# Kernel optimization log

Measured on AMD Instinct MI355X. Metric: run time of the kernel, lower is better.

The kernel has to match this reference:

```python
import jax, jax.numpy as jnp
import numpy as np

N_ATOMS = 20000
HIDDEN = 128
N_ITERS = 2
BATCH = 16
N_BONDS = 60000


def setup_inputs() -> dict:
    key = jax.random.key(0)
    k1, k2, k3, k4, k5, k6 = jax.random.split(key, 6)
    positions = jax.random.normal(k1, (BATCH, N_ATOMS, 3), dtype=jnp.float32)
    bonds = jax.random.randint(k2, (N_BONDS, 2), 0, N_ATOMS, dtype=jnp.int32)
    # nn.Linear(3, 128): weight [128,3], bias [128] -> store transposed for x @ W
    W_msg = jax.random.normal(k3, (3, HIDDEN), dtype=jnp.float32) / jnp.sqrt(3.0)
    b_msg = jax.random.normal(k4, (HIDDEN,), dtype=jnp.float32) * 0.01
    # nn.Linear(128, 3)
    W_upd = jax.random.normal(k5, (HIDDEN, 3), dtype=jnp.float32) / jnp.sqrt(float(HIDDEN))
    b_upd = jax.random.normal(k6, (3,), dtype=jnp.float32) * 0.01
    return {"positions": positions, "bonds": bonds,
            "W_msg": W_msg, "b_msg": b_msg, "W_upd": W_upd, "b_upd": b_upd}


def reference(positions, bonds, W_msg, b_msg, W_upd, b_upd):
    B, N, _ = positions.shape
    # Bidirectional edges: message flows src -> dst (adj_list[dst] contains src).
    src = jnp.concatenate([bonds[:, 0], bonds[:, 1]])  # [2E]
    dst = jnp.concatenate([bonds[:, 1], bonds[:, 0]])  # [2E]
    deg = jnp.zeros((N,), jnp.float32).at[dst].add(1.0)  # in-degree per atom
    inv_deg = jnp.where(deg > 0, 1.0 / jnp.maximum(deg, 1.0), 0.0)  # [N]

    h = positions
    for _ in range(N_ITERS):
        node_msg = h @ W_msg + b_msg                      # [B,N,H] msg_linear per node
        gathered = node_msg[:, src, :]                    # [B,2E,H]
        agg = jnp.zeros((B, N, HIDDEN), h.dtype).at[:, dst, :].add(gathered)  # sum per dst
        msgs = agg * inv_deg[None, :, None]               # mean over neighbors (0 if isolated)
        h = h + (msgs @ W_upd + b_upd)                    # update_linear + residual
    return h
```

## Files before the change

kernel.cpp:

```cpp
#include <hip/hip_runtime.h>

#define N_ATOMS 20000
#define BATCH   16
#define N_BONDS 60000
#define NB      (N_ATOMS * BATCH)
#define CAP     32

#define TRANS_BLOCKS 1250
#define DEG_BLOCKS   235
#define NGROUPS      1250

#define OFF_CNT   0
#define OFF_MC    20000
#define OFF_ADJF  20016
#define OFF_POST  (OFF_ADJF + N_ATOMS * CAP)
#define OFF_H2T   (OFF_POST + NB * 2)

__device__ __forceinline__ unsigned short f2bf(float f) {
    unsigned int u = __float_as_uint(f);
    u += 0x7FFFu + ((u >> 16) & 1u);
    return (unsigned short)(u >> 16);
}
__device__ __forceinline__ float bf2f(unsigned short h) {
    return __uint_as_float(((unsigned int)h) << 16);
}

__global__ void build_kernel(const float* __restrict__ pos, const int* __restrict__ bonds,
                             const float* __restrict__ W_msg, const float* __restrict__ b_msg,
                             const float* __restrict__ W_upd,
                             int* __restrict__ cnt, int* __restrict__ adjF,
                             float* __restrict__ Mc, ushort4* __restrict__ posT) {
    int blk = blockIdx.x;
    if (blk < TRANS_BLOCKS) {
        int t = blk * 256 + threadIdx.x;
        int b = t & 15, n = t >> 4;
        const float* p = pos + ((size_t)b * N_ATOMS + n) * 3;
        posT[n * 16 + b] = make_ushort4(f2bf(p[0]), f2bf(p[1]), f2bf(p[2]), 0);
    } else if (blk < TRANS_BLOCKS + DEG_BLOCKS) {
        int e = (blk - TRANS_BLOCKS) * 256 + threadIdx.x;
        if (e < N_BONDS) {
            int a0 = bonds[2 * e], a1 = bonds[2 * e + 1];
            int s0 = atomicAdd(&cnt[a0], 1);
            if (s0 < CAP) adjF[a0 * CAP + s0] = a1;
            int s1 = atomicAdd(&cnt[a1], 1);
            if (s1 < CAP) adjF[a1 * CAP + s1] = a0;
        }
    } else {
        int t = threadIdx.x;
        if (t < 12) {
            float s = 0.0f;
            if (t < 9) {
                int i = t / 3, j = t % 3;
                for (int k = 0; k < 128; ++k) s += W_msg[i * 128 + k] * W_upd[k * 3 + j];
            } else {
                int j = t - 9;
                for (int k = 0; k < 128; ++k) s += b_msg[k] * W_upd[k * 3 + j];
            }
            Mc[t] = s;
        }
    }
}

template <bool FINAL>
__global__ __launch_bounds__(256) void gather_kernel(const ushort4* __restrict__ hT,
                                                     const int* __restrict__ cnt,
                                                     const int* __restrict__ adjF,
                                                     const float* __restrict__ Mc,
                                                     const float* __restrict__ b_upd,
                                                     ushort4* __restrict__ outT,
                                                     float* __restrict__ outP) {
    __shared__ float lds[16 * 51];
    int t = threadIdx.x;
    int b = t & 15;
    int nl = t >> 4;
    int n = blockIdx.x * 16 + nl;
    const int4* al4 = (const int4*)(adjF + n * CAP);
    int dc = cnt[n];
    int d = dc > CAP ? CAP : dc;
    int4 ja = al4[0];
    int4 jb = al4[1];
    ushort4 mh = hT[n * 16 + b];
    float sx = 0.0f, sy = 0.0f, sz = 0.0f;
#define ACC(J) { ushort4 v = hT[(size_t)(J) * 16 + b]; \
                 sx += bf2f(v.x); sy += bf2f(v.y); sz += bf2f(v.z); }
    if (0 < d) ACC(ja.x)
    if (1 < d) ACC(ja.y)
    if (2 < d) ACC(ja.z)
    if (3 < d) ACC(ja.w)
    if (4 < d) ACC(jb.x)
    if (5 < d) ACC(jb.y)
    if (6 < d) ACC(jb.z)
    if (7 < d) ACC(jb.w)
    for (int k0 = 8; k0 < d; k0 += 8) {
        ja = al4[k0 >> 2];
        jb = al4[(k0 >> 2) + 1];
        if (k0 + 0 < d) ACC(ja.x)
        if (k0 + 1 < d) ACC(ja.y)
        if (k0 + 2 < d) ACC(ja.z)
        if (k0 + 3 < d) ACC(ja.w)
        if (k0 + 4 < d) ACC(jb.x)
        if (k0 + 5 < d) ACC(jb.y)
        if (k0 + 6 < d) ACC(jb.z)
        if (k0 + 7 < d) ACC(jb.w)
    }
#undef ACC
    float mex = bf2f(mh.x), mey = bf2f(mh.y), mez = bf2f(mh.z);
    float inv = d > 0 ? 1.0f / (float)d : 0.0f;
    float flag = d > 0 ? 1.0f : 0.0f;
    float o0 = mex + inv * (sx * Mc[0] + sy * Mc[3] + sz * Mc[6]) + flag * Mc[9]  + b_upd[0];
    float o1 = mey + inv * (sx * Mc[1] + sy * Mc[4] + sz * Mc[7]) + flag * Mc[10] + b_upd[1];
    float o2 = mez + inv * (sx * Mc[2] + sy * Mc[5] + sz * Mc[8]) + flag * Mc[11] + b_upd[2];
    if (!FINAL) {
        outT[n * 16 + b] = make_ushort4(f2bf(o0), f2bf(o1), f2bf(o2), 0);
    } else {
        lds[nl * 51 + b * 3 + 0] = o0;
        lds[nl * 51 + b * 3 + 1] = o1;
        lds[nl * 51 + b * 3 + 2] = o2;
        __syncthreads();
        int b2 = t >> 4, n2 = t & 15;
        float* op = outP + ((size_t)b2 * N_ATOMS + (size_t)(blockIdx.x * 16 + n2)) * 3;
        op[0] = lds[n2 * 51 + b2 * 3 + 0];
        op[1] = lds[n2 * 51 + b2 * 3 + 1];
        op[2] = lds[n2 * 51 + b2 * 3 + 2];
    }
}

extern "C" void kernel_launch(void* const* d_in, const int* in_sizes, int n_in,
                              void* d_out, int out_size, void* d_ws, size_t ws_size,
                              hipStream_t stream) {
    const float* positions = (const float*)d_in[0];
    const int* bonds = (const int*)d_in[1];
    const float* W_msg = (const float*)d_in[2];
    const float* b_msg = (const float*)d_in[3];
    const float* W_upd = (const float*)d_in[4];
    const float* b_upd = (const float*)d_in[5];
    float* out = (float*)d_out;

    int* wsi = (int*)d_ws;
    int* cnt = wsi + OFF_CNT;
    float* Mc = (float*)(wsi + OFF_MC);
    int* adjF = wsi + OFF_ADJF;
    ushort4* posT = (ushort4*)(wsi + OFF_POST);
    ushort4* h2T = (ushort4*)(wsi + OFF_H2T);

    hipMemsetAsync(cnt, 0, N_ATOMS * sizeof(int), stream);
    build_kernel<<<TRANS_BLOCKS + DEG_BLOCKS + 1, 256, 0, stream>>>(
        positions, bonds, W_msg, b_msg, W_upd, cnt, adjF, Mc, posT);
    gather_kernel<false><<<NGROUPS, 256, 0, stream>>>(posT, cnt, adjF, Mc, b_upd, h2T, nullptr);
    gather_kernel<true><<<NGROUPS, 256, 0, stream>>>(h2T, cnt, adjF, Mc, b_upd, nullptr, out);
}
```

Baseline: 38.50 us.

## Fuse two message-passing iterations into one 2-hop gather kernel

```diff
diff --git a/kernel.cpp b/kernel.cpp
--- a/kernel.cpp
+++ b/kernel.cpp
@@ -8,13 +8,11 @@
 
 #define TRANS_BLOCKS 1250
 #define DEG_BLOCKS   235
-#define NGROUPS      1250
 
 #define OFF_CNT   0
 #define OFF_MC    20000
-#define OFF_ADJF  20016
+#define OFF_ADJF  20024
 #define OFF_POST  (OFF_ADJF + N_ATOMS * CAP)
-#define OFF_H2T   (OFF_POST + NB * 2)
 
 __device__ __forceinline__ unsigned short f2bf(float f) {
     unsigned int u = __float_as_uint(f);
@@ -27,7 +25,7 @@
 
 __global__ void build_kernel(const float* __restrict__ pos, const int* __restrict__ bonds,
                              const float* __restrict__ W_msg, const float* __restrict__ b_msg,
-                             const float* __restrict__ W_upd,
+                             const float* __restrict__ W_upd, const float* __restrict__ b_upd,
                              int* __restrict__ cnt, int* __restrict__ adjF,
                              float* __restrict__ Mc, ushort4* __restrict__ posT) {
     int blk = blockIdx.x;
@@ -46,6 +44,7 @@
             if (s1 < CAP) adjF[a1 * CAP + s1] = a0;
         }
     } else {
+        __shared__ float sm[12];
         int t = threadIdx.x;
         if (t < 12) {
             float s = 0.0f;
@@ -56,73 +55,109 @@
                 int j = t - 9;
                 for (int k = 0; k < 128; ++k) s += b_msg[k] * W_upd[k * 3 + j];
             }
-            Mc[t] = s;
+            sm[t] = s;
+        }
+        __syncthreads();
+        if (t < 9) {
+            int i = t / 3, j = t % 3;
+            Mc[t] = sm[t];
+            float s = 0.0f;
+            for (int k = 0; k < 3; ++k) s += sm[i * 3 + k] * sm[k * 3 + j];
+            Mc[9 + t] = s;
+        } else if (t < 12) {
+            int j = t - 9;
+            float s = 0.0f;
+            for (int k = 0; k < 3; ++k) s += (sm[9 + k] + b_upd[k]) * sm[k * 3 + j];
+            Mc[18 + j] = s + 2.0f * sm[9 + j];
         }
     }
 }
 
-template <bool FINAL>
-__global__ __launch_bounds__(256) void gather_kernel(const ushort4* __restrict__ hT,
-                                                     const int* __restrict__ cnt,
-                                                     const int* __restrict__ adjF,
-                                                     const float* __restrict__ Mc,
-                                                     const float* __restrict__ b_upd,
-                                                     ushort4* __restrict__ outT,
-                                                     float* __restrict__ outP) {
-    __shared__ float lds[16 * 51];
+__global__ __launch_bounds__(128) void gather2_kernel(const ushort4* __restrict__ hT,
+                                                      const int* __restrict__ cnt,
+                                                      const int* __restrict__ adjF,
+                                                      const float* __restrict__ Mc,
+                                                      const float* __restrict__ b_upd,
+                                                      float* __restrict__ outP) {
+    __shared__ float lds[8 * 51];
     int t = threadIdx.x;
     int b = t & 15;
     int nl = t >> 4;
-    int n = blockIdx.x * 16 + nl;
+    int n = blockIdx.x * 8 + nl;
     const int4* al4 = (const int4*)(adjF + n * CAP);
-    int dc = cnt[n];
-    int d = dc > CAP ? CAP : dc;
+    int dn = cnt[n];
+    if (dn > CAP) dn = CAP;
     int4 ja = al4[0];
     int4 jb = al4[1];
     ushort4 mh = hT[n * 16 + b];
-    float sx = 0.0f, sy = 0.0f, sz = 0.0f;
-#define ACC(J) { ushort4 v = hT[(size_t)(J) * 16 + b]; \
-                 sx += bf2f(v.x); sy += bf2f(v.y); sz += bf2f(v.z); }
-    if (0 < d) ACC(ja.x)
-    if (1 < d) ACC(ja.y)
-    if (2 < d) ACC(ja.z)
-    if (3 < d) ACC(ja.w)
-    if (4 < d) ACC(jb.x)
-    if (5 < d) ACC(jb.y)
-    if (6 < d) ACC(jb.z)
-    if (7 < d) ACC(jb.w)
-    for (int k0 = 8; k0 < d; k0 += 8) {
-        ja = al4[k0 >> 2];
-        jb = al4[(k0 >> 2) + 1];
-        if (k0 + 0 < d) ACC(ja.x)
-        if (k0 + 1 < d) ACC(ja.y)
-        if (k0 + 2 < d) ACC(ja.z)
-        if (k0 + 3 < d) ACC(ja.w)
-        if (k0 + 4 < d) ACC(jb.x)
-        if (k0 + 5 < d) ACC(jb.y)
-        if (k0 + 6 < d) ACC(jb.z)
-        if (k0 + 7 < d) ACC(jb.w)
+    float S1x = 0.f, S1y = 0.f, S1z = 0.f;
+    float S2x = 0.f, S2y = 0.f, S2z = 0.f;
+    int js[8] = {ja.x, ja.y, ja.z, ja.w, jb.x, jb.y, jb.z, jb.w};
+#pragma unroll
+    for (int i = 0; i < 8; ++i) {
+        if (i < dn) {
+            int j = js[i];
+            int dj = cnt[j];
+            if (dj > CAP) dj = CAP;
+            const int4* jl4 = (const int4*)(adjF + j * CAP);
+            int4 ka = jl4[0];
+            int4 kb = jl4[1];
+            ushort4 hj = hT[(size_t)j * 16 + b];
+            S1x += bf2f(hj.x); S1y += bf2f(hj.y); S1z += bf2f(hj.z);
+            int ks[8] = {ka.x, ka.y, ka.z, ka.w, kb.x, kb.y, kb.z, kb.w};
+            float Tx = 0.f, Ty = 0.f, Tz = 0.f;
+#pragma unroll
+            for (int q = 0; q < 8; ++q) {
+                if (q < dj) {
+                    ushort4 hk = hT[(size_t)ks[q] * 16 + b];
+                    Tx += bf2f(hk.x); Ty += bf2f(hk.y); Tz += bf2f(hk.z);
+                }
+            }
+            for (int q = 8; q < dj; ++q) {
+                int kk = adjF[j * CAP + q];
+                ushort4 hk = hT[(size_t)kk * 16 + b];
+                Tx += bf2f(hk.x); Ty += bf2f(hk.y); Tz += bf2f(hk.z);
+            }
+            float invj = 1.0f / (float)dj;
+            S2x += invj * Tx; S2y += invj * Ty; S2z += invj * Tz;
+        }
     }
-#undef ACC
-    float mex = bf2f(mh.x), mey = bf2f(mh.y), mez = bf2f(mh.z);
-    float inv = d > 0 ? 1.0f / (float)d : 0.0f;
-    float flag = d > 0 ? 1.0f : 0.0f;
-    float o0 = mex + inv * (sx * Mc[0] + sy * Mc[3] + sz * Mc[6]) + flag * Mc[9]  + b_upd[0];
-    float o1 = mey + inv * (sx * Mc[1] + sy * Mc[4] + sz * Mc[7]) + flag * Mc[10] + b_upd[1];
-    float o2 = mez + inv * (sx * Mc[2] + sy * Mc[5] + sz * Mc[8]) + flag * Mc[11] + b_upd[2];
-    if (!FINAL) {
-        outT[n * 16 + b] = make_ushort4(f2bf(o0), f2bf(o1), f2bf(o2), 0);
-    } else {
-        lds[nl * 51 + b * 3 + 0] = o0;
-        lds[nl * 51 + b * 3 + 1] = o1;
-        lds[nl * 51 + b * 3 + 2] = o2;
-        __syncthreads();
-        int b2 = t >> 4, n2 = t & 15;
-        float* op = outP + ((size_t)b2 * N_ATOMS + (size_t)(blockIdx.x * 16 + n2)) * 3;
-        op[0] = lds[n2 * 51 + b2 * 3 + 0];
-        op[1] = lds[n2 * 51 + b2 * 3 + 1];
-        op[2] = lds[n2 * 51 + b2 * 3 + 2];
+    for (int i = 8; i < dn; ++i) {
+        int j = adjF[n * CAP + i];
+        int dj = cnt[j];
+        if (dj > CAP) dj = CAP;
+        ushort4 hj = hT[(size_t)j * 16 + b];
+        S1x += bf2f(hj.x); S1y += bf2f(hj.y); S1z += bf2f(hj.z);
+        float Tx = 0.f, Ty = 0.f, Tz = 0.f;
+        for (int q = 0; q < dj; ++q) {
+            int kk = adjF[j * CAP + q];
+            ushort4 hk = hT[(size_t)kk * 16 + b];
+            Tx += bf2f(hk.x); Ty += bf2f(hk.y); Tz += bf2f(hk.z);
+        }
+        float invj = 1.0f / (float)dj;
+        S2x += invj * Tx; S2y += invj * Ty; S2z += invj * Tz;
     }
+    float inv = dn > 0 ? 1.0f / (float)dn : 0.0f;
+    float flag = dn > 0 ? 1.0f : 0.0f;
+    float A1x = 2.f * S1x, A1y = 2.f * S1y, A1z = 2.f * S1z;
+    float o0 = bf2f(mh.x) + inv * (A1x * Mc[0] + A1y * Mc[3] + A1z * Mc[6]
+                                 + S2x * Mc[9] + S2y * Mc[12] + S2z * Mc[15])
+             + flag * Mc[18] + 2.f * b_upd[0];
+    float o1 = bf2f(mh.y) + inv * (A1x * Mc[1] + A1y * Mc[4] + A1z * Mc[7]
+                                 + S2x * Mc[10] + S2y * Mc[13] + S2z * Mc[16])
+             + flag * Mc[19] + 2.f * b_upd[1];
+    float o2 = bf2f(mh.z) + inv * (A1x * Mc[2] + A1y * Mc[5] + A1z * Mc[8]
+                                 + S2x * Mc[11] + S2y * Mc[14] + S2z * Mc[17])
+             + flag * Mc[20] + 2.f * b_upd[2];
+    lds[nl * 51 + b * 3 + 0] = o0;
+    lds[nl * 51 + b * 3 + 1] = o1;
+    lds[nl * 51 + b * 3 + 2] = o2;
+    __syncthreads();
+    int b2 = t >> 3, n2 = t & 7;
+    float* op = outP + ((size_t)b2 * N_ATOMS + (size_t)(blockIdx.x * 8 + n2)) * 3;
+    op[0] = lds[n2 * 51 + b2 * 3 + 0];
+    op[1] = lds[n2 * 51 + b2 * 3 + 1];
+    op[2] = lds[n2 * 51 + b2 * 3 + 2];
 }
 
 extern "C" void kernel_launch(void* const* d_in, const int* in_sizes, int n_in,
@@ -141,11 +176,9 @@
     float* Mc = (float*)(wsi + OFF_MC);
     int* adjF = wsi + OFF_ADJF;
     ushort4* posT = (ushort4*)(wsi + OFF_POST);
-    ushort4* h2T = (ushort4*)(wsi + OFF_H2T);
 
     hipMemsetAsync(cnt, 0, N_ATOMS * sizeof(int), stream);
     build_kernel<<<TRANS_BLOCKS + DEG_BLOCKS + 1, 256, 0, stream>>>(
-        positions, bonds, W_msg, b_msg, W_upd, cnt, adjF, Mc, posT);
-    gather_kernel<false><<<NGROUPS, 256, 0, stream>>>(posT, cnt, adjF, Mc, b_upd, h2T, nullptr);
-    gather_kernel<true><<<NGROUPS, 256, 0, stream>>>(h2T, cnt, adjF, Mc, b_upd, nullptr, out);
+        positions, bonds, W_msg, b_msg, W_upd, b_upd, cnt, adjF, Mc, posT);
+    gather2_kernel<<<N_ATOMS / 8, 128, 0, stream>>>(posT, cnt, adjF, Mc, b_upd, out);
 }
```

New measurement: 73.58 us. +91.1%, slower.
